# Kernel tuning notes

Hardware: AMD Instinct MI355X
Metric: run time of the kernel (lower is better)

Reference implementation:

```python
import jax, jax.numpy as jnp
import numpy as np

N_TOKENS = 8192
IN_FEATURES = 4096
OUT_FEATURES = 4096


def setup_inputs() -> dict:
    key = jax.random.key(0)
    kx, kw, ks = jax.random.split(key, 3)
    x = jax.random.normal(kx, (N_TOKENS, IN_FEATURES), dtype=jnp.float32)
    # int8 weight in [-127, 126], per torch.randint(-127, 127, ...)
    weight = jax.random.randint(kw, (OUT_FEATURES, IN_FEATURES), -127, 127, dtype=jnp.int32).astype(jnp.int8)
    weight_scales = jax.random.uniform(ks, (OUT_FEATURES,), dtype=jnp.float32, minval=0.001, maxval=0.01)
    bias = jnp.zeros((1, OUT_FEATURES), dtype=jnp.float32)
    return {"x": x, "weight": weight, "weight_scales": weight_scales, "bias": bias}


def reference(x, weight, weight_scales, bias):
    # --- dynamic per-token activation quantization (min-max / abs-max) ---
    # scale per token so that max |x| maps to 127
    x_absmax = jnp.max(jnp.abs(x), axis=-1, keepdims=True)          # [T, 1]
    x_scale = x_absmax / 127.0                                       # [T, 1]
    q_x = jnp.clip(jnp.round(x / x_scale), -127, 127).astype(jnp.int8)  # [T, K]

    # --- int8 GEMM with int32 accumulation: q_y = q_x @ weight.T ---
    q_y = jax.lax.dot_general(
        q_x, weight,
        dimension_numbers=(((1,), (1,)), ((), ())),
        preferred_element_type=jnp.int32,
    )                                                                # [T, N] int32

    # --- dequantize: per-channel weight scale x per-token activation scale ---
    y = q_y.astype(jnp.float32) * weight_scales[None, :] * x_scale   # [T, N]
    y = y + bias
    return y
```

## Files before the change

### kernel.cpp

```cpp
#include <hip/hip_runtime.h>
#include <cstdint>
#include <cstddef>

#define T_TOKENS 8192
#define K_DIM 4096
#define N_DIM 4096

using i32x4 = __attribute__((ext_vector_type(4))) int;

__global__ __launch_bounds__(256) void pack_weight(const int* __restrict__ win,
                                                   int8_t* __restrict__ wout) {
    const int idx = blockIdx.x * 256 + threadIdx.x;
    const i32x4 v = reinterpret_cast<const i32x4*>(win)[idx];
    uint32_t pk = (uint32_t)(v.x & 255) | ((uint32_t)(v.y & 255) << 8) |
                  ((uint32_t)(v.z & 255) << 16) | ((uint32_t)(v.w & 255) << 24);
    reinterpret_cast<int*>(wout)[idx] = (int)pk;
}

__global__ __launch_bounds__(256) void quant_rows(const float* __restrict__ x,
                                                  int8_t* __restrict__ qx,
                                                  float* __restrict__ xscale) {
    const int t = blockIdx.x;
    const int tid = threadIdx.x;
    const float4* row = reinterpret_cast<const float4*>(x + (size_t)t * K_DIM);

    float4 v[4];
    float amax = 0.0f;
#pragma unroll
    for (int i = 0; i < 4; ++i) {
        v[i] = row[i * 256 + tid];
        amax = fmaxf(amax, fabsf(v[i].x));
        amax = fmaxf(amax, fabsf(v[i].y));
        amax = fmaxf(amax, fabsf(v[i].z));
        amax = fmaxf(amax, fabsf(v[i].w));
    }
#pragma unroll
    for (int off = 32; off > 0; off >>= 1)
        amax = fmaxf(amax, __shfl_xor(amax, off));

    __shared__ float red[4];
    if ((tid & 63) == 0) red[tid >> 6] = amax;
    __syncthreads();
    amax = fmaxf(fmaxf(red[0], red[1]), fmaxf(red[2], red[3]));

    const float scale = fmaxf(amax, 1e-30f) * (1.0f / 127.0f);
    if (tid == 0) xscale[t] = scale;

    int* qrow = reinterpret_cast<int*>(qx + (size_t)t * K_DIM);
#pragma unroll
    for (int i = 0; i < 4; ++i) {
        int q0 = (int)fminf(fmaxf(rintf(v[i].x / scale), -127.0f), 127.0f);
        int q1 = (int)fminf(fmaxf(rintf(v[i].y / scale), -127.0f), 127.0f);
        int q2 = (int)fminf(fmaxf(rintf(v[i].z / scale), -127.0f), 127.0f);
        int q3 = (int)fminf(fmaxf(rintf(v[i].w / scale), -127.0f), 127.0f);
        uint32_t pk = (uint32_t)(q0 & 255) | ((uint32_t)(q1 & 255) << 8) |
                      ((uint32_t)(q2 & 255) << 16) | ((uint32_t)(q3 & 255) << 24);
        qrow[i * 256 + tid] = (int)pk;
    }
}

__global__ __launch_bounds__(256) void int8_gemm(const int8_t* __restrict__ qx,
                                                 const int8_t* __restrict__ w,
                                                 const float* __restrict__ xscale,
                                                 const float* __restrict__ wscale,
                                                 const float* __restrict__ bias,
                                                 float* __restrict__ out) {
    __shared__ int8_t As[128 * 64];
    __shared__ int8_t Bs[128 * 64];

    const int tid = threadIdx.x;
    const int lane = tid & 63;
    const int wave = tid >> 6;
    const int wr = wave >> 1;
    const int wc = wave & 1;
    const int l16 = lane & 15;
    const int quad = lane >> 4;

    const size_t a_row0 = (size_t)blockIdx.x * 128;
    const size_t b_row0 = (size_t)blockIdx.y * 128;

    const int s_row = tid >> 2;
    const int s_col = (tid & 3) * 16;

    const int8_t* ag0 = qx + (a_row0 + s_row) * (size_t)K_DIM + s_col;
    const int8_t* ag1 = ag0 + (size_t)64 * K_DIM;
    const int8_t* bg0 = w + (b_row0 + s_row) * (size_t)K_DIM + s_col;
    const int8_t* bg1 = bg0 + (size_t)64 * K_DIM;

    i32x4* As4 = reinterpret_cast<i32x4*>(As);
    i32x4* Bs4 = reinterpret_cast<i32x4*>(Bs);

    i32x4 acc[4][4] = {};

    i32x4 ra0 = *reinterpret_cast<const i32x4*>(ag0);
    i32x4 ra1 = *reinterpret_cast<const i32x4*>(ag1);
    i32x4 rb0 = *reinterpret_cast<const i32x4*>(bg0);
    i32x4 rb1 = *reinterpret_cast<const i32x4*>(bg1);

    for (int k0 = 0; k0 < K_DIM; k0 += 64) {
        __syncthreads();
        As4[tid] = ra0;
        As4[tid + 256] = ra1;
        Bs4[tid] = rb0;
        Bs4[tid + 256] = rb1;
        __syncthreads();

        const int k1 = k0 + 64;
        if (k1 < K_DIM) {
            ra0 = *reinterpret_cast<const i32x4*>(ag0 + k1);
            ra1 = *reinterpret_cast<const i32x4*>(ag1 + k1);
            rb0 = *reinterpret_cast<const i32x4*>(bg0 + k1);
            rb1 = *reinterpret_cast<const i32x4*>(bg1 + k1);
        }

        i32x4 af[4], bf[4];
#pragma unroll
        for (int i = 0; i < 4; ++i) {
            af[i] = As4[((wr * 64 + i * 16 + l16) * 64 + quad * 16) >> 4];
            bf[i] = Bs4[((wc * 64 + i * 16 + l16) * 64 + quad * 16) >> 4];
        }
#pragma unroll
        for (int i = 0; i < 4; ++i)
#pragma unroll
            for (int j = 0; j < 4; ++j)
                acc[i][j] = __builtin_amdgcn_mfma_i32_16x16x64_i8(af[i], bf[j], acc[i][j], 0, 0, 0);
    }

#pragma unroll
    for (int j = 0; j < 4; ++j) {
        const int n = (int)b_row0 + wc * 64 + j * 16 + l16;
        const float ws = wscale[n];
        const float bs = bias[n];
#pragma unroll
        for (int i = 0; i < 4; ++i) {
#pragma unroll
            for (int r = 0; r < 4; ++r) {
                const int t = (int)a_row0 + wr * 64 + i * 16 + quad * 4 + r;
                const float xs = xscale[t];
                out[(size_t)t * N_DIM + n] = (float)acc[i][j][r] * ws * xs + bs;
            }
        }
    }
}

extern "C" void kernel_launch(void* const* d_in, const int* in_sizes, int n_in,
                              void* d_out, int out_size, void* d_ws, size_t ws_size,
                              hipStream_t stream) {
    const float* x = (const float*)d_in[0];
    const int* w_i32 = (const int*)d_in[1];
    const float* wscale = (const float*)d_in[2];
    const float* bias = (const float*)d_in[3];
    float* out = (float*)d_out;

    int8_t* qx = (int8_t*)d_ws;
    float* xscale = (float*)((char*)d_ws + (size_t)T_TOKENS * K_DIM);
    int8_t* wpk = (int8_t*)((char*)d_ws + (size_t)T_TOKENS * K_DIM + 65536);

    pack_weight<<<(N_DIM * K_DIM / 4) / 256, 256, 0, stream>>>(w_i32, wpk);

    quant_rows<<<T_TOKENS, 256, 0, stream>>>(x, qx, xscale);

    dim3 grid(T_TOKENS / 128, N_DIM / 128);
    int8_gemm<<<grid, 256, 0, stream>>>(qx, wpk, xscale, wscale, bias, out);
}
```

Measured before the change: 474.8 us.

## Load GEMM tiles directly into LDS with global_load_lds and fragment-major layout

Replaces register-staged global loads and LDS stores in the int8 GEMM with direct global-to-LDS loads via the global_load_lds builtin. The LDS tile is rearranged to a fragment-major layout so each lane reads its MFMA fragment contiguously, which is meant to avoid bank conflicts and cut VGPR use. The register prefetch of the next K tile is dropped, so loads are no longer overlapped with MFMA work. There is also no explicit wait for the async LDS writes beyond the __syncthreads, which is a correctness risk unless the compiler inserts vmcnt waits.

```diff
diff --git a/kernel.cpp b/kernel.cpp
--- a/kernel.cpp
+++ b/kernel.cpp
@@ -7,6 +7,12 @@
 #define N_DIM 4096
 
 using i32x4 = __attribute__((ext_vector_type(4))) int;
+
+__device__ __forceinline__ void glds16(const int8_t* g, int8_t* l) {
+    __builtin_amdgcn_global_load_lds(
+        (const __attribute__((address_space(1))) unsigned int*)g,
+        (__attribute__((address_space(3))) unsigned int*)l, 16, 0, 0);
+}
 
 __global__ __launch_bounds__(256) void pack_weight(const int* __restrict__ win,
                                                    int8_t* __restrict__ wout) {
@@ -79,45 +85,34 @@
     const size_t a_row0 = (size_t)blockIdx.x * 128;
     const size_t b_row0 = (size_t)blockIdx.y * 128;
 
-    const int s_row = tid >> 2;
-    const int s_col = (tid & 3) * 16;
+    const int8_t* agA = qx + (a_row0 + wave * 16 + l16) * (size_t)K_DIM + quad * 16;
+    const int8_t* agB = agA + (size_t)64 * K_DIM;
+    const int8_t* bgA = w + (b_row0 + wave * 16 + l16) * (size_t)K_DIM + quad * 16;
+    const int8_t* bgB = bgA + (size_t)64 * K_DIM;
 
-    const int8_t* ag0 = qx + (a_row0 + s_row) * (size_t)K_DIM + s_col;
-    const int8_t* ag1 = ag0 + (size_t)64 * K_DIM;
-    const int8_t* bg0 = w + (b_row0 + s_row) * (size_t)K_DIM + s_col;
-    const int8_t* bg1 = bg0 + (size_t)64 * K_DIM;
+    int8_t* ldsA0 = As + tid * 16;
+    int8_t* ldsA1 = As + 4096 + tid * 16;
+    int8_t* ldsB0 = Bs + tid * 16;
+    int8_t* ldsB1 = Bs + 4096 + tid * 16;
 
     i32x4* As4 = reinterpret_cast<i32x4*>(As);
     i32x4* Bs4 = reinterpret_cast<i32x4*>(Bs);
 
     i32x4 acc[4][4] = {};
 
-    i32x4 ra0 = *reinterpret_cast<const i32x4*>(ag0);
-    i32x4 ra1 = *reinterpret_cast<const i32x4*>(ag1);
-    i32x4 rb0 = *reinterpret_cast<const i32x4*>(bg0);
-    i32x4 rb1 = *reinterpret_cast<const i32x4*>(bg1);
-
     for (int k0 = 0; k0 < K_DIM; k0 += 64) {
         __syncthreads();
-        As4[tid] = ra0;
-        As4[tid + 256] = ra1;
-        Bs4[tid] = rb0;
-        Bs4[tid + 256] = rb1;
+        glds16(agA + k0, ldsA0);
+        glds16(agB + k0, ldsA1);
+        glds16(bgA + k0, ldsB0);
+        glds16(bgB + k0, ldsB1);
         __syncthreads();
-
-        const int k1 = k0 + 64;
-        if (k1 < K_DIM) {
-            ra0 = *reinterpret_cast<const i32x4*>(ag0 + k1);
-            ra1 = *reinterpret_cast<const i32x4*>(ag1 + k1);
-            rb0 = *reinterpret_cast<const i32x4*>(bg0 + k1);
-            rb1 = *reinterpret_cast<const i32x4*>(bg1 + k1);
-        }
 
         i32x4 af[4], bf[4];
 #pragma unroll
         for (int i = 0; i < 4; ++i) {
-            af[i] = As4[((wr * 64 + i * 16 + l16) * 64 + quad * 16) >> 4];
-            bf[i] = Bs4[((wc * 64 + i * 16 + l16) * 64 + quad * 16) >> 4];
+            af[i] = As4[(wr * 4 + i) * 64 + lane];
+            bf[i] = Bs4[(wc * 4 + i) * 64 + lane];
         }
 #pragma unroll
         for (int i = 0; i < 4; ++i)
@@ -157,7 +152,6 @@
     int8_t* wpk = (int8_t*)((char*)d_ws + (size_t)T_TOKENS * K_DIM + 65536);
 
     pack_weight<<<(N_DIM * K_DIM / 4) / 256, 256, 0, stream>>>(w_i32, wpk);
-
     quant_rows<<<T_TOKENS, 256, 0, stream>>>(x, qx, xscale);
 
     dim3 grid(T_TOKENS / 128, N_DIM / 128);
```

Measured after the change: 540.7 us. 1.14x slower.
